# Optimization experiments

Measured on AMD Instinct MI355X. Metric: run time of the kernel, lower is better.

The kernel has to match this reference:

```python
import jax, jax.numpy as jnp
import numpy as np

B, N, V, D, L = 8, 2048, 256, 512, 6
H, DH = 8, 64
INNER = H * DH          # 512
WSZ = 128               # local attention window
NW = N // WSZ           # 16 windows (N multiple of WSZ -> autopad no-op)
FF = int(D * 4 * 2 / 3) # 1365 GEGLU inner dim
SCALE = DH ** -0.5
DPB = D // 2            # dynamic position bias MLP width


def _ln(x, g, b):
    m = x.mean(-1, keepdims=True)
    v = ((x - m) ** 2).mean(-1, keepdims=True)
    return (x - m) * jax.lax.rsqrt(v + 1e-5) * g + b


def _pos_emb(n, d):
    inv = 1.0 / (10000.0 ** (jnp.arange(0, d, 2, dtype=jnp.float32) / d))
    s = jnp.arange(n, dtype=jnp.float32)[:, None] * inv[None, :]
    return jnp.concatenate([jnp.sin(s), jnp.cos(s)], axis=-1)  # (n, d)


def _look(t, pad_val):
    # t: (..., NW, WSZ, c) -> (..., NW, 2*WSZ, c): [previous window, current window]
    prev = jnp.concatenate([jnp.full_like(t[..., :1, :, :], pad_val), t[..., :-1, :, :]], axis=-3)
    return jnp.concatenate([prev, t], axis=-2)


def _dpb_bias(w1, b1, w2, b2, w3, b3):
    # DynamicPositionBias(i=WSZ, j=2*WSZ) -> (H, WSZ, 2*WSZ)
    rel = jnp.arange(2 * WSZ, dtype=jnp.float32)[:, None]
    h = jax.nn.silu(rel @ w1 + b1)
    h = jax.nn.silu(h @ w2 + b2)
    tab = h @ w3 + b3                       # (2*WSZ, H)
    iseq = jnp.arange(WSZ, 2 * WSZ)
    jseq = jnp.arange(2 * WSZ)
    idx = jnp.abs(iseq[:, None] - jseq[None, :])  # (WSZ, 2*WSZ)
    return jnp.transpose(tab[idx], (2, 0, 1))


def setup_inputs():
    key = jax.random.key(0)
    ks = jax.random.split(key, 12)
    nrm = lambda k, shape, s=0.02: jax.random.normal(k, shape, dtype=jnp.float32) * s
    emb = nrm(ks[1], (V, D), 1.0).at[0].set(0.0)  # padding_idx=0 row zeroed
    return dict(
        x=jax.random.randint(ks[0], (B, N), 0, V),
        emb=emb,
        ln_attn_g=jnp.ones((L, D)), ln_attn_b=jnp.zeros((L, D)),
        w_qkv=nrm(ks[2], (L, D, 3 * INNER)),
        w_out=nrm(ks[3], (L, INNER, D)),
        ln_ff_g=jnp.ones((L, D)), ln_ff_b=jnp.zeros((L, D)),
        w_ff1=nrm(ks[4], (L, D, 2 * FF)),
        w_ff2=nrm(ks[5], (L, FF, D)),
        dpb_w1=nrm(ks[6], (1, DPB), 0.5), dpb_b1=jnp.zeros((DPB,)),
        dpb_w2=nrm(ks[7], (DPB, DPB), 0.05), dpb_b2=jnp.zeros((DPB,)),
        dpb_w3=nrm(ks[8], (DPB, H), 0.05), dpb_b3=jnp.zeros((H,)),
        ln_out_g=jnp.ones((D,)), ln_out_b=jnp.zeros((D,)),
        w_logits=nrm(ks[9], (D, D)),
    )


def _forward(x, emb, ln_attn_g, ln_attn_b, w_qkv, w_out, ln_ff_g, ln_ff_b,
             w_ff1, w_ff2, dpb_w1, dpb_b1, dpb_w2, dpb_b2, dpb_w3, dpb_b3,
             ln_out_g, ln_out_b, w_logits):
    mask = x != 0                                  # padding mask (B, N)
    h = emb[x] * mask[..., None] + _pos_emb(N, D)[None]
    bias = _dpb_bias(dpb_w1, dpb_b1, dpb_w2, dpb_b2, dpb_w3, dpb_b3)  # (H, w, 2w)
    pos = jnp.arange(N).reshape(NW, WSZ)
    kpos = _look(pos[None, :, :, None], -1)[0, :, :, 0]               # (NW, 2w)
    # causal mask + exact-windowsize clip + left pad mask (shared over batch/heads)
    inval = (pos[:, :, None] < kpos[:, None, :]) | (pos[:, :, None] > kpos[:, None, :] + WSZ) | (kpos[:, None, :] == -1)
    kmask = _look(mask.reshape(B, NW, WSZ)[..., None], False)[..., 0]  # (B, NW, 2w)
    neg = -jnp.finfo(jnp.float32).max

    def towin(t):  # (B, N, INNER) -> (B, H, NW, WSZ, DH)
        return t.reshape(B, N, H, DH).transpose(0, 2, 1, 3).reshape(B, H, NW, WSZ, DH)

    def layer(hx, p):
        lg, lb, wqkv, wout, fg, fb, w1, w2 = p
        # local windowed attention: look_backward=1, look_forward=0, causal
        z = _ln(hx, lg, lb)
        q, k, v = map(towin, jnp.split(z @ wqkv, 3, axis=-1))
        k2, v2 = _look(k, -1.0), _look(v, -1.0)   # pad_value=-1 (masked below)
        sim = jnp.einsum('bhwid,bhwjd->bhwij', q * SCALE, k2) + bias[None, :, None]
        sim = jnp.where(inval[None, None], neg, sim)
        sim = jnp.where(kmask[:, None, :, None, :], sim, neg)
        a = jax.nn.softmax(sim, axis=-1)
        o = jnp.einsum('bhwij,bhwjd->bhwid', a, v2)
        o = o.reshape(B, H, N, DH).transpose(0, 2, 1, 3).reshape(B, N, INNER)
        hx = hx + o @ wout
        # GEGLU feed-forward
        u = _ln(hx, fg, fb) @ w1
        a1, g1 = jnp.split(u, 2, axis=-1)
        hx = hx + (a1 * jax.nn.gelu(g1, approximate=False)) @ w2
        return hx, None

    h, _ = jax.lax.scan(layer, h, (ln_attn_g, ln_attn_b, w_qkv, w_out, ln_ff_g, ln_ff_b, w_ff1, w_ff2))
    return _ln(h, ln_out_g, ln_out_b) @ w_logits   # (B, N, D)


def reference(x, emb, ln_attn_g, ln_attn_b, w_qkv, w_out, ln_ff_g, ln_ff_b,
              w_ff1, w_ff2, dpb_w1, dpb_b1, dpb_w2, dpb_b2, dpb_w3, dpb_b3,
              ln_out_g, ln_out_b, w_logits):
    return _forward(x, emb, ln_attn_g, ln_attn_b, w_qkv, w_out, ln_ff_g, ln_ff_b,
                    w_ff1, w_ff2, dpb_w1, dpb_b1, dpb_w2, dpb_b2, dpb_w3, dpb_b3,
                    ln_out_g, ln_out_b, w_logits)
```

## Files before the change

### kernel.cpp

```cpp
#include <hip/hip_runtime.h>
#include <hip/hip_bf16.h>
#include <math.h>

typedef __hip_bfloat16 bf16;
typedef __attribute__((ext_vector_type(8))) short short8;
typedef __attribute__((ext_vector_type(4))) float floatx4;

#define NEG_MAX 3.402823466e38f

__device__ __forceinline__ void gload16(const void* g, void* l) {
  __builtin_amdgcn_global_load_lds(
      (const __attribute__((address_space(1))) unsigned int*)g,
      (__attribute__((address_space(3))) unsigned int*)l, 16, 0, 0);
}
__device__ __forceinline__ floatx4 mfma_bf16(short8 a, short8 b, floatx4 c) {
  return __builtin_amdgcn_mfma_f32_16x16x32_bf16(a, b, c, 0, 0, 0);
}

__global__ __launch_bounds__(256) void prep_w(const float* __restrict__ src,
                                              bf16* __restrict__ dst,
                                              int K, int N, int pK, int pN, int nl, int mode) {
  int idx = blockIdx.x * 256 + threadIdx.x;
  long total = (long)nl * pN * pK;
  if (idx >= total) return;
  int l = idx / (pN * pK);
  int r = idx % (pN * pK);
  int n = r / pK, k = r % pK;
  const float* s = src + (size_t)l * K * N;
  float v = 0.f;
  if (k < K) {
    int sc = -1;
    if (mode == 0) { if (n < N) sc = n; }
    else { if (n < 1365) sc = n; else if (n >= 1408 && n < 2773) sc = 1365 + (n - 1408); }
    if (sc >= 0) v = s[(size_t)k * N + sc];
  }
  dst[idx] = __float2bfloat16(v);
}

__global__ __launch_bounds__(256) void dpb_kernel(const float* w1, const float* b1,
                                                  const float* w2, const float* b2,
                                                  const float* w3, const float* b3,
                                                  float* __restrict__ tab) {
  __shared__ float h1[256];
  __shared__ float h2s[256];
  int t = blockIdx.x, e = threadIdx.x;
  float rel = (float)t;
  float a = rel * w1[e] + b1[e];
  h1[e] = a / (1.f + expf(-a));
  __syncthreads();
  float s = b2[e];
  for (int d = 0; d < 256; d++) s += h1[d] * w2[d * 256 + e];
  h2s[e] = s / (1.f + expf(-s));
  __syncthreads();
  if (e < 8) {
    float s2 = b3[e];
    for (int d = 0; d < 256; d++) s2 += h2s[d] * w3[d * 8 + e];
    tab[t * 8 + e] = s2;
  }
}

__global__ __launch_bounds__(256) void embed_kernel(const int* __restrict__ x,
                                                    const float* __restrict__ emb,
                                                    float* __restrict__ h) {
  int idx = blockIdx.x * 256 + threadIdx.x;
  int bn = idx >> 9, d = idx & 511;
  int n = bn & 2047;
  int xv = x[bn];
  float e = (xv != 0) ? emb[(size_t)xv * 512 + d] : 0.f;
  int k = d & 255;
  float inv = powf(10000.f, -(float)k * (1.f / 256.f));
  float s = (float)n * inv;
  float pe = (d < 256) ? sinf(s) : cosf(s);
  h[idx] = e + pe;
}

__global__ __launch_bounds__(256) void ln_kernel(const float* __restrict__ h,
                                                 const float* __restrict__ g,
                                                 const float* __restrict__ b,
                                                 bf16* __restrict__ z) {
  int wv = threadIdx.x >> 6, lane = threadIdx.x & 63;
  size_t row = (size_t)blockIdx.x * 4 + wv;
  const float* xr = h + row * 512;
  float v[8];
  float s = 0.f;
#pragma unroll
  for (int i = 0; i < 8; i++) { v[i] = xr[lane * 8 + i]; s += v[i]; }
#pragma unroll
  for (int o = 32; o > 0; o >>= 1) s += __shfl_xor(s, o);
  float mean = s * (1.f / 512.f);
  float q = 0.f;
#pragma unroll
  for (int i = 0; i < 8; i++) { float d = v[i] - mean; q += d * d; }
#pragma unroll
  for (int o = 32; o > 0; o >>= 1) q += __shfl_xor(q, o);
  float rs = rsqrtf(q * (1.f / 512.f) + 1e-5f);
  bf16* zr = z + row * 512;
#pragma unroll
  for (int i = 0; i < 8; i++) {
    int col = lane * 8 + i;
    float o2 = (v[i] - mean) * rs * g[col] + b[col];
    zr[col] = __float2bfloat16(o2);
  }
}

template <int EPI>
__global__ __launch_bounds__(256, 2) void gemm_kernel(const bf16* __restrict__ A,
                                                      const bf16* __restrict__ BT,
                                                      bf16* __restrict__ Cb,
                                                      float* __restrict__ Cf,
                                                      int Nsz, int Ksz) {
  __shared__ __align__(16) char smem[32768];
  const int tid = threadIdx.x, wv = tid >> 6, lane = tid & 63;
  const int lr = lane & 15, lg = lane >> 4;
  const int m0 = blockIdx.y * 128, n0 = blockIdx.x * 128;
  const int wm = (wv >> 1) * 64, wn = (wv & 1) * 64;
  const size_t Kb = (size_t)Ksz * 2;

  floatx4 acc[4][4];
#pragma unroll
  for (int i = 0; i < 4; i++)
#pragma unroll
    for (int j = 0; j < 4; j++)
#pragma unroll
      for (int r = 0; r < 4; r++) acc[i][j][r] = 0.f;

  for (int kt = 0; kt < Ksz; kt += 64) {
#pragma unroll
    for (int i = 0; i < 4; i++) {
      int off = i * 4096 + wv * 1024 + lane * 16;
      int row = off >> 7, colb = off & 127;
      int scol = colb ^ ((row & 7) << 4);
      gload16((const char*)A + (size_t)(m0 + row) * Kb + (size_t)kt * 2 + scol, smem + off);
    }
#pragma unroll
    for (int i = 0; i < 4; i++) {
      int off = i * 4096 + wv * 1024 + lane * 16;
      int row = off >> 7, colb = off & 127;
      int scol = colb ^ ((row & 7) << 4);
      gload16((const char*)BT + (size_t)(n0 + row) * Kb + (size_t)kt * 2 + scol,
              smem + 16384 + off);
    }
    __syncthreads();
#pragma unroll
    for (int kk = 0; kk < 64; kk += 32) {
      int kb = kk * 2 + lg * 16;
      short8 af[4], bfr[4];
#pragma unroll
      for (int mf = 0; mf < 4; mf++) {
        int row = wm + mf * 16 + lr;
        af[mf] = *(const short8*)(smem + row * 128 + (kb ^ ((row & 7) << 4)));
      }
#pragma unroll
      for (int nf = 0; nf < 4; nf++) {
        int row = wn + nf * 16 + lr;
        bfr[nf] = *(const short8*)(smem + 16384 + row * 128 + (kb ^ ((row & 7) << 4)));
      }
#pragma unroll
      for (int mf = 0; mf < 4; mf++)
#pragma unroll
        for (int nf = 0; nf < 4; nf++) acc[mf][nf] = mfma_bf16(af[mf], bfr[nf], acc[mf][nf]);
    }
    __syncthreads();
  }
#pragma unroll
  for (int mf = 0; mf < 4; mf++)
#pragma unroll
    for (int nf = 0; nf < 4; nf++)
#pragma unroll
      for (int r = 0; r < 4; r++) {
        int row = m0 + wm + mf * 16 + lg * 4 + r;
        int col = n0 + wn + nf * 16 + lr;
        float v = acc[mf][nf][r];
        size_t idx = (size_t)row * Nsz + col;
        if (EPI == 0) {
          Cb[idx] = __float2bfloat16(v);
        } else if (EPI == 1) {
          Cf[idx] += v;
        } else if (EPI == 2) {
          float a = __bfloat162float(Cb[idx]);
          float ge = 0.5f * v * (1.f + erff(v * 0.70710678118654752f));
          Cb[idx] = __float2bfloat16(a * ge);
        } else {
          Cf[idx] = v;
        }
      }
}

__global__ __launch_bounds__(256) void attn_kernel(const bf16* __restrict__ qkv,
                                                   const int* __restrict__ x,
                                                   const float* __restrict__ tab,
                                                   bf16* __restrict__ ob) {
  __shared__ __align__(16) char smem[51200];
  float* km = (float*)(smem + 49152);
  float* tabh = (float*)(smem + 50176);
  const int w2 = blockIdx.x, hh = blockIdx.y, b = blockIdx.z;
  const int w = w2 >> 1, qh = (w2 & 1) * 64;
  const int tid = threadIdx.x, wv = tid >> 6, lane = tid & 63;
  const int lr = lane & 15, lg = lane >> 4;
  const size_t qrow0 = (size_t)b * 2048 + (size_t)w * 128;

  for (int c = tid; c < 2048; c += 256) {
    int j = c >> 3, d0 = (c & 7) * 8;
    short8 vv;
    if (w == 0 && j < 128) {
#pragma unroll
      for (int t2 = 0; t2 < 8; t2++) vv[t2] = (short)0xBF80;
    } else {
      size_t gj = qrow0 + j - 128;
      vv = *(const short8*)(qkv + gj * 1536 + 1024 + hh * 64 + d0);
    }
#pragma unroll
    for (int t2 = 0; t2 < 8; t2++) {
      int d = d0 + t2;
      *(unsigned short*)(smem + 16384 + d * 512 + ((j * 2) ^ ((d & 7) << 4))) =
          (unsigned short)vv[t2];
    }
  }
  {
    tabh[tid] = tab[tid * 8 + hh];
    int j = tid;
    float kmv;
    if (w == 0 && j < 128) kmv = 0.f;
    else kmv = (x[qrow0 + j - 128] != 0) ? 1.f : 0.f;
    km[j] = kmv;
  }
  __syncthreads();

  floatx4 sim[16];
#pragma unroll
  for (int nf = 0; nf < 16; nf++)
#pragma unroll
    for (int r = 0; r < 4; r++) sim[nf][r] = 0.f;
#pragma unroll
  for (int kk = 0; kk < 64; kk += 32) {
    size_t qr = qrow0 + qh + wv * 16 + lr;
    short8 bq = *(const short8*)(qkv + qr * 1536 + hh * 64 + kk + lg * 8);
#pragma unroll
    for (int nf = 0; nf < 16; nf++) {
      int j = nf * 16 + lr;
      size_t gj = (w == 0 && j < 128) ? qrow0 : (qrow0 + j - 128);
      short8 ak = *(const short8*)(qkv + gj * 1536 + 512 + hh * 64 + kk + lg * 8);
      sim[nf] = mfma_bf16(ak, bq, sim[nf]);
    }
  }
  const int qi = qh + wv * 16 + lr;
  float mmax = -NEG_MAX;
#pragma unroll
  for (int nf = 0; nf < 16; nf++)
#pragma unroll
    for (int r = 0; r < 4; r++) {
      int jj = nf * 16 + lg * 4 + r;
      int di = 128 + qi - jj;
      if (di < 0) di = -di;
      float val = sim[nf][r] * 0.125f + tabh[di];
      bool causal = (nf < 8) ? (qi <= jj) : (jj - 128 <= qi);
      bool valid = causal && (km[jj] > 0.5f);
      float mv = valid ? val : -NEG_MAX;
      sim[nf][r] = mv;
      mmax = fmaxf(mmax, mv);
    }
  mmax = fmaxf(mmax, __shfl_xor(mmax, 16));
  mmax = fmaxf(mmax, __shfl_xor(mmax, 32));
  float lsum = 0.f;
#pragma unroll
  for (int nf = 0; nf < 16; nf++)
#pragma unroll
    for (int r = 0; r < 4; r++) {
      float e = __expf(sim[nf][r] - mmax);
      sim[nf][r] = e;
      lsum += e;
    }
  lsum += __shfl_xor(lsum, 16);
  lsum += __shfl_xor(lsum, 32);
  float inv_l = 1.f / lsum;

  floatx4 oacc[4];
#pragma unroll
  for (int nf = 0; nf < 4; nf++)
#pragma unroll
    for (int r = 0; r < 4; r++) oacc[nf][r] = 0.f;

  const int ql = wv * 16 + lr;
#pragma unroll
  for (int t = 0; t < 2; t++) {
#pragma unroll
    for (int nfl = 0; nfl < 8; nfl++) {
      int nf = t * 8 + nfl;
      unsigned int lo = (unsigned int)__bfloat16_as_ushort(__float2bfloat16(sim[nf][0])) |
                        ((unsigned int)__bfloat16_as_ushort(__float2bfloat16(sim[nf][1])) << 16);
      unsigned int hi = (unsigned int)__bfloat16_as_ushort(__float2bfloat16(sim[nf][2])) |
                        ((unsigned int)__bfloat16_as_ushort(__float2bfloat16(sim[nf][3])) << 16);
      uint2 pk; pk.x = lo; pk.y = hi;
      int bo = nfl * 32 + lg * 8;
      *(uint2*)(smem + ql * 256 + (bo ^ ((ql & 7) << 4))) = pk;
    }
    __syncthreads();
#pragma unroll
    for (int kkl = 0; kkl < 128; kkl += 32) {
      int bo = kkl * 2 + lg * 16;
      short8 pa = *(const short8*)(smem + ql * 256 + (bo ^ ((ql & 7) << 4)));
      int vb = t * 256 + bo;
#pragma unroll
      for (int nf = 0; nf < 4; nf++) {
        int d = nf * 16 + lr;
        short8 bv = *(const short8*)(smem + 16384 + d * 512 + (vb ^ ((d & 7) << 4)));
        oacc[nf] = mfma_bf16(pa, bv, oacc[nf]);
      }
    }
    __syncthreads();
  }
  float invq[4];
#pragma unroll
  for (int r = 0; r < 4; r++) invq[r] = __shfl(inv_l, (lane & 48) | (lg * 4 + r));
#pragma unroll
  for (int nf = 0; nf < 4; nf++)
#pragma unroll
    for (int r = 0; r < 4; r++) {
      size_t n = qrow0 + qh + wv * 16 + lg * 4 + r;
      ob[n * 512 + hh * 64 + nf * 16 + lr] = __float2bfloat16(oacc[nf][r] * invq[r]);
    }
}

extern "C" void kernel_launch(void* const* d_in, const int* in_sizes, int n_in,
                              void* d_out, int out_size, void* d_ws, size_t ws_size,
                              hipStream_t stream) {
  const int* x = (const int*)d_in[0];
  const float* emb = (const float*)d_in[1];
  const float* lag = (const float*)d_in[2];
  const float* lab = (const float*)d_in[3];
  const float* wqkv = (const float*)d_in[4];
  const float* wout = (const float*)d_in[5];
  const float* lfg = (const float*)d_in[6];
  const float* lfb = (const float*)d_in[7];
  const float* wff1 = (const float*)d_in[8];
  const float* wff2 = (const float*)d_in[9];
  const float* dw1 = (const float*)d_in[10];
  const float* db1 = (const float*)d_in[11];
  const float* dw2 = (const float*)d_in[12];
  const float* db2 = (const float*)d_in[13];
  const float* dw3 = (const float*)d_in[14];
  const float* db3 = (const float*)d_in[15];
  const float* log_g = (const float*)d_in[16];
  const float* log_b = (const float*)d_in[17];
  const float* wlog = (const float*)d_in[18];

  char* ws = (char*)d_ws;
  size_t off = 0;
  float* h = (float*)(ws + off); off += (size_t)16384 * 512 * 4;
  bf16* z = (bf16*)(ws + off); off += (size_t)16384 * 512 * 2;
  bf16* ob = z;
  bf16* big = (bf16*)(ws + off); off += (size_t)16384 * 1536 * 2;
  bf16* qkvT = (bf16*)(ws + off); off += (size_t)6 * 1536 * 512 * 2;
  bf16* woutT = (bf16*)(ws + off); off += (size_t)6 * 512 * 512 * 2;
  bf16* ff1T = (bf16*)(ws + off); off += (size_t)6 * 2816 * 512 * 2;
  bf16* ff2T = (bf16*)(ws + off); off += (size_t)6 * 512 * 1408 * 2;
  bf16* logT = (bf16*)(ws + off); off += (size_t)512 * 512 * 2;
  float* tab = (float*)(ws + off); off += (size_t)256 * 8 * 4;

  auto cdiv = [](long t) { return (int)((t + 255) / 256); };

  prep_w<<<cdiv(6L * 1536 * 512), 256, 0, stream>>>(wqkv, qkvT, 512, 1536, 512, 1536, 6, 0);
  prep_w<<<cdiv(6L * 512 * 512), 256, 0, stream>>>(wout, woutT, 512, 512, 512, 512, 6, 0);
  prep_w<<<cdiv(6L * 2816 * 512), 256, 0, stream>>>(wff1, ff1T, 512, 2730, 512, 2816, 6, 1);
  prep_w<<<cdiv(6L * 512 * 1408), 256, 0, stream>>>(wff2, ff2T, 1365, 512, 1408, 512, 6, 0);
  prep_w<<<cdiv(512L * 512), 256, 0, stream>>>(wlog, logT, 512, 512, 512, 512, 1, 0);
  dpb_kernel<<<256, 256, 0, stream>>>(dw1, db1, dw2, db2, dw3, db3, tab);
  embed_kernel<<<32768, 256, 0, stream>>>(x, emb, h);

  for (int l = 0; l < 6; l++) {
    ln_kernel<<<4096, 256, 0, stream>>>(h, lag + l * 512, lab + l * 512, z);
    gemm_kernel<0><<<dim3(12, 128), 256, 0, stream>>>(z, qkvT + (size_t)l * 1536 * 512,
                                                      big, nullptr, 1536, 512);
    attn_kernel<<<dim3(32, 8, 8), 256, 0, stream>>>(big, x, tab, ob);
    gemm_kernel<1><<<dim3(4, 128), 256, 0, stream>>>(ob, woutT + (size_t)l * 512 * 512,
                                                     nullptr, h, 512, 512);
    ln_kernel<<<4096, 256, 0, stream>>>(h, lfg + l * 512, lfb + l * 512, z);
    gemm_kernel<0><<<dim3(11, 128), 256, 0, stream>>>(z, ff1T + (size_t)l * 2816 * 512,
                                                      big, nullptr, 1408, 512);
    gemm_kernel<2><<<dim3(11, 128), 256, 0, stream>>>(
        z, ff1T + (size_t)l * 2816 * 512 + (size_t)1408 * 512, big, nullptr, 1408, 512);
    gemm_kernel<1><<<dim3(4, 128), 256, 0, stream>>>(big, ff2T + (size_t)l * 512 * 1408,
                                                     nullptr, h, 512, 1408);
  }
  ln_kernel<<<4096, 256, 0, stream>>>(h, log_g, log_b, z);
  gemm_kernel<3><<<dim3(4, 128), 256, 0, stream>>>(z, logT, nullptr, (float*)d_out, 512, 512);
}
```

Measured before the change: 2.132 ms.

## Add 256x256-tile double-buffered GEMM for QKV and FF1 projections

```diff
diff --git a/kernel.cpp b/kernel.cpp
--- a/kernel.cpp
+++ b/kernel.cpp
@@ -31,7 +31,7 @@
   if (k < K) {
     int sc = -1;
     if (mode == 0) { if (n < N) sc = n; }
-    else { if (n < 1365) sc = n; else if (n >= 1408 && n < 2773) sc = 1365 + (n - 1408); }
+    else { if (n < 1365) sc = n; else if (n >= 1536 && n < 2901) sc = 1365 + (n - 1536); }
     if (sc >= 0) v = s[(size_t)k * N + sc];
   }
   dst[idx] = __float2bfloat16(v);
@@ -176,12 +176,120 @@
           Cb[idx] = __float2bfloat16(v);
         } else if (EPI == 1) {
           Cf[idx] += v;
-        } else if (EPI == 2) {
-          float a = __bfloat162float(Cb[idx]);
-          float ge = 0.5f * v * (1.f + erff(v * 0.70710678118654752f));
-          Cb[idx] = __float2bfloat16(a * ge);
         } else {
           Cf[idx] = v;
+        }
+      }
+}
+
+template <int EPI>
+__global__ __launch_bounds__(512, 1) void gemm256_kernel(const bf16* __restrict__ A,
+                                                         const bf16* __restrict__ BT,
+                                                         bf16* __restrict__ Cb,
+                                                         int Nstride, int Nreal, int Ksz) {
+  __shared__ __align__(16) char smem[131072];
+  const int tid = threadIdx.x;
+  const int lane = tid & 63, lr = lane & 15, lg = lane >> 4;
+  const int wid = tid >> 6;
+  const int gridN = gridDim.x;
+  const int nwg = gridN << 6;
+  const int linear = blockIdx.y * gridN + blockIdx.x;
+  const int swz = (linear & 7) * (nwg >> 3) + (linear >> 3);
+  const int m0 = (swz / gridN) * 256, n0 = (swz % gridN) * 256;
+  const int wrow = (wid >> 2) * 128, wcol = (wid & 3) * 64;
+  const size_t Kb = (size_t)Ksz * 2;
+  const int nt = Ksz >> 6;
+
+  floatx4 acc[8][4];
+#pragma unroll
+  for (int i = 0; i < 8; i++)
+#pragma unroll
+    for (int j = 0; j < 4; j++)
+#pragma unroll
+      for (int r = 0; r < 4; r++) acc[i][j][r] = 0.f;
+
+  auto stage_half = [&](int t, int h) {
+    const char* src = (const char*)((h < 2) ? A : BT);
+    const int rbase = ((h < 2) ? m0 : n0) + (h & 1) * 128;
+    char* dst = smem + (t & 1) * 65536 + h * 16384;
+    const size_t kt2 = (size_t)t * 128;
+#pragma unroll
+    for (int i = 0; i < 2; i++) {
+      int off = i * 8192 + tid * 16;
+      int row = off >> 7, colb = off & 127;
+      gload16(src + (size_t)(rbase + row) * Kb + kt2 + (colb ^ ((row & 7) << 4)), dst + off);
+    }
+  };
+
+  stage_half(0, 0); stage_half(0, 1); stage_half(0, 2); stage_half(0, 3);
+  asm volatile("s_waitcnt vmcnt(0)" ::: "memory");
+  __builtin_amdgcn_s_barrier();
+  __builtin_amdgcn_sched_barrier(0);
+
+  for (int t = 0; t < nt; ++t) {
+    const int cb = (t & 1) << 16;
+#pragma unroll
+    for (int q = 0; q < 4; ++q) {
+      const int qm = q & 1, qn = q >> 1;
+      short8 af[2][4], bv[2][2];
+#pragma unroll
+      for (int kx = 0; kx < 2; ++kx) {
+        const int kb = kx * 64 + lg * 16;
+#pragma unroll
+        for (int m = 0; m < 4; ++m) {
+          int arow = wrow + (qm * 4 + m) * 16 + lr;
+          af[kx][m] = *(const short8*)(smem + cb + ((arow >> 7) << 14) +
+                                       ((arow & 127) << 7) + (kb ^ ((arow & 7) << 4)));
+        }
+#pragma unroll
+        for (int n = 0; n < 2; ++n) {
+          int brow = wcol + (qn * 2 + n) * 16 + lr;
+          bv[kx][n] = *(const short8*)(smem + cb + 32768 + ((brow >> 7) << 14) +
+                                       ((brow & 127) << 7) + (kb ^ ((brow & 7) << 4)));
+        }
+      }
+      if (t + 1 < nt) {
+        if (q == 0) { stage_half(t + 1, 0); stage_half(t + 1, 1); }
+        else if (q == 1) { stage_half(t + 1, 2); stage_half(t + 1, 3); }
+      }
+      __builtin_amdgcn_sched_barrier(0);
+      __builtin_amdgcn_s_barrier();
+      asm volatile("s_waitcnt lgkmcnt(0)" ::: "memory");
+      __builtin_amdgcn_sched_barrier(0);
+      __builtin_amdgcn_s_setprio(1);
+#pragma unroll
+      for (int kx = 0; kx < 2; ++kx)
+#pragma unroll
+        for (int m = 0; m < 4; ++m)
+#pragma unroll
+          for (int n = 0; n < 2; ++n)
+            acc[qm * 4 + m][qn * 2 + n] =
+                mfma_bf16(af[kx][m], bv[kx][n], acc[qm * 4 + m][qn * 2 + n]);
+      __builtin_amdgcn_s_setprio(0);
+      __builtin_amdgcn_sched_barrier(0);
+      if (q == 3) asm volatile("s_waitcnt vmcnt(0)" ::: "memory");
+      __builtin_amdgcn_s_barrier();
+      __builtin_amdgcn_sched_barrier(0);
+    }
+  }
+#pragma unroll
+  for (int mf = 0; mf < 8; ++mf)
+#pragma unroll
+    for (int nf = 0; nf < 4; ++nf)
+#pragma unroll
+      for (int r = 0; r < 4; ++r) {
+        int col = n0 + wcol + nf * 16 + lr;
+        if (col < Nreal) {
+          int row = m0 + wrow + mf * 16 + lg * 4 + r;
+          float v = acc[mf][nf][r];
+          size_t idx = (size_t)row * Nstride + col;
+          if (EPI == 0) {
+            Cb[idx] = __float2bfloat16(v);
+          } else {
+            float a = __bfloat162float(Cb[idx]);
+            float ge = 0.5f * v * (1.f + erff(v * 0.70710678118654752f));
+            Cb[idx] = __float2bfloat16(a * ge);
+          }
         }
       }
 }
@@ -352,7 +460,7 @@
   bf16* big = (bf16*)(ws + off); off += (size_t)16384 * 1536 * 2;
   bf16* qkvT = (bf16*)(ws + off); off += (size_t)6 * 1536 * 512 * 2;
   bf16* woutT = (bf16*)(ws + off); off += (size_t)6 * 512 * 512 * 2;
-  bf16* ff1T = (bf16*)(ws + off); off += (size_t)6 * 2816 * 512 * 2;
+  bf16* ff1T = (bf16*)(ws + off); off += (size_t)6 * 3072 * 512 * 2;
   bf16* ff2T = (bf16*)(ws + off); off += (size_t)6 * 512 * 1408 * 2;
   bf16* logT = (bf16*)(ws + off); off += (size_t)512 * 512 * 2;
   float* tab = (float*)(ws + off); off += (size_t)256 * 8 * 4;
@@ -361,7 +469,7 @@
 
   prep_w<<<cdiv(6L * 1536 * 512), 256, 0, stream>>>(wqkv, qkvT, 512, 1536, 512, 1536, 6, 0);
   prep_w<<<cdiv(6L * 512 * 512), 256, 0, stream>>>(wout, woutT, 512, 512, 512, 512, 6, 0);
-  prep_w<<<cdiv(6L * 2816 * 512), 256, 0, stream>>>(wff1, ff1T, 512, 2730, 512, 2816, 6, 1);
+  prep_w<<<cdiv(6L * 3072 * 512), 256, 0, stream>>>(wff1, ff1T, 512, 2730, 512, 3072, 6, 1);
   prep_w<<<cdiv(6L * 512 * 1408), 256, 0, stream>>>(wff2, ff2T, 1365, 512, 1408, 512, 6, 0);
   prep_w<<<cdiv(512L * 512), 256, 0, stream>>>(wlog, logT, 512, 512, 512, 512, 1, 0);
   dpb_kernel<<<256, 256, 0, stream>>>(dw1, db1, dw2, db2, dw3, db3, tab);
@@ -369,16 +477,16 @@
 
   for (int l = 0; l < 6; l++) {
     ln_kernel<<<4096, 256, 0, stream>>>(h, lag + l * 512, lab + l * 512, z);
-    gemm_kernel<0><<<dim3(12, 128), 256, 0, stream>>>(z, qkvT + (size_t)l * 1536 * 512,
-                                                      big, nullptr, 1536, 512);
+    gemm256_kernel<0><<<dim3(6, 64), 512, 0, stream>>>(z, qkvT + (size_t)l * 1536 * 512,
+                                                       big, 1536, 1536, 512);
     attn_kernel<<<dim3(32, 8, 8), 256, 0, stream>>>(big, x, tab, ob);
     gemm_kernel<1><<<dim3(4, 128), 256, 0, stream>>>(ob, woutT + (size_t)l * 512 * 512,
                                                      nullptr, h, 512, 512);
     ln_kernel<<<4096, 256, 0, stream>>>(h, lfg + l * 512, lfb + l * 512, z);
-    gemm_kernel<0><<<dim3(11, 128), 256, 0, stream>>>(z, ff1T + (size_t)l * 2816 * 512,
-                                                      big, nullptr, 1408, 512);
-    gemm_kernel<2><<<dim3(11, 128), 256, 0, stream>>>(
-        z, ff1T + (size_t)l * 2816 * 512 + (size_t)1408 * 512, big, nullptr, 1408, 512);
+    gemm256_kernel<0><<<dim3(6, 64), 512, 0, stream>>>(z, ff1T + (size_t)l * 3072 * 512,
+                                                       big, 1408, 1408, 512);
+    gemm256_kernel<2><<<dim3(6, 64), 512, 0, stream>>>(
+        z, ff1T + (size_t)l * 3072 * 512 + (size_t)1536 * 512, big, 1408, 1408, 512);
     gemm_kernel<1><<<dim3(4, 128), 256, 0, stream>>>(big, ff2T + (size_t)l * 512 * 1408,
                                                      nullptr, h, 512, 1408);
   }
```

Result: slower. 2.447 ms (+14.8%).
